# Optimization experiments

Hardware: AMD Instinct MI355X
Metric: run time of the kernel (lower is better)

## Reference

```python
import jax, jax.numpy as jnp
import numpy as np

# irreps layout: in/out = 32x0e + 8x1o  (dim 32 + 24 = 56), sh = 1x0e + 1x1o (dim 4)
NS, NV = 32, 8
N_NODES, N_EDGES, N_EDGE_FEAT, HIDDEN = 10000, 100000, 64, 64
W_NUMEL = NS*NS + NS*NV + NV*NV + NV*NS  # 1600
EPS = 1e-5
# path normalization (e3nn-style 'component'/'element'):
# fan_in into 0e output = 32 (0x0 path) + 8 (1x1 path) = 40; same for 1o output.
INV40 = 1.0 / np.sqrt(40.0)            # paths with trivial/identity CG net factor
INV120 = 1.0 / np.sqrt(120.0)          # paths with w3j = delta/sqrt(3) extra factor


def setup_inputs() -> dict:
    key = jax.random.key(0)
    ks = jax.random.split(key, 12)
    node_attr = jax.random.normal(ks[0], (N_NODES, 56), dtype=jnp.float32)
    edge_attr = jax.random.normal(ks[1], (N_EDGES, N_EDGE_FEAT), dtype=jnp.float32)
    edge_sh = jax.random.normal(ks[2], (N_EDGES, 4), dtype=jnp.float32)
    edge_index = jax.random.randint(ks[3], (2, N_EDGES), 0, N_NODES, dtype=jnp.int64)
    s1 = 1.0 / np.sqrt(N_EDGE_FEAT)
    s2 = 1.0 / np.sqrt(HIDDEN)
    fc1_w = jax.random.normal(ks[4], (N_EDGE_FEAT, HIDDEN), dtype=jnp.float32) * s1
    fc1_b = jnp.zeros((HIDDEN,), dtype=jnp.float32)
    fc2_w = jax.random.normal(ks[5], (HIDDEN, W_NUMEL), dtype=jnp.float32) * s2
    fc2_b = jnp.zeros((W_NUMEL,), dtype=jnp.float32)
    bn_gamma0 = jnp.ones((NS,), dtype=jnp.float32)
    bn_beta0 = jnp.zeros((NS,), dtype=jnp.float32)
    bn_gamma1 = jnp.ones((NV,), dtype=jnp.float32)
    return dict(node_attr=node_attr, edge_attr=edge_attr, edge_sh=edge_sh,
                edge_index=edge_index, fc1_w=fc1_w, fc1_b=fc1_b,
                fc2_w=fc2_w, fc2_b=fc2_b, bn_gamma0=bn_gamma0,
                bn_beta0=bn_beta0, bn_gamma1=bn_gamma1)


def _forward(node_attr, edge_attr, edge_sh, fc1_w, fc1_b, fc2_w, fc2_b,
             bn_gamma0, bn_beta0, bn_gamma1, edge_index):
    E = edge_attr.shape[0]
    N = node_attr.shape[0]
    edge_src, edge_dst = edge_index[0], edge_index[1]

    # edge MLP -> per-edge tensor-product weights [E, 1600]
    h = jax.nn.relu(edge_attr @ fc1_w + fc1_b)
    w = h @ fc2_w + fc2_b
    o1 = NS * NS            # 0e x 0e -> 0e
    o2 = o1 + NS * NV       # 0e x 1o -> 1o
    o3 = o2 + NV * NV       # 1o x 0e -> 1o
    w00 = w[:, :o1].reshape(E, NS, NS)
    w01 = w[:, o1:o2].reshape(E, NS, NV)
    w10 = w[:, o2:o3].reshape(E, NV, NV)
    w11 = w[:, o3:].reshape(E, NV, NS)

    # gather node features at destination, split into scalar / vector irreps
    x = node_attr[edge_dst]                  # [E, 56]
    x0 = x[:, :NS]                           # [E, 32] scalars
    x1 = x[:, NS:].reshape(E, NV, 3)         # [E, 8, 3] l=1 vectors
    s0 = edge_sh[:, 0]                       # [E]
    s1 = edge_sh[:, 1:4]                     # [E, 3]

    # Clebsch-Gordan paths (w3j(1,1,0)=w3j(1,0,1)=w3j(0,1,1)=delta/sqrt(3))
    out0 = jnp.einsum('eu,euw->ew', x0 * s0[:, None], w00) * INV40 \
         + jnp.einsum('eui,ei,euw->ew', x1, s1, w11) * INV120
    out1 = jnp.einsum('eu,ei,euw->ewi', x0, s1, w01) * INV40 \
         + jnp.einsum('eui,euw->ewi', x1 * s0[:, None, None], w10) * INV40
    tp_out = jnp.concatenate([out0, out1.reshape(E, NV * 3)], axis=-1)  # [E, 56]

    # scatter-mean over edge_src
    sums = jax.ops.segment_sum(tp_out, edge_src, num_segments=N)
    cnt = jax.ops.segment_sum(jnp.ones((E,), tp_out.dtype), edge_src, num_segments=N)
    out = sums / jnp.maximum(cnt, 1.0)[:, None]

    # residual (in_dim == out_dim, pad is a no-op)
    out = out + node_attr

    # e3nn-style BatchNorm (training statistics, reduce='mean')
    sc = out[:, :NS]
    vec = out[:, NS:].reshape(N, NV, 3)
    m = sc.mean(axis=0)
    sc_c = sc - m
    var = (sc_c ** 2).mean(axis=0)
    sc_n = sc_c * jax.lax.rsqrt(var + EPS) * bn_gamma0 + bn_beta0
    vnorm = (vec ** 2).mean(axis=-1).mean(axis=0)          # [NV]
    vec_n = vec * (jax.lax.rsqrt(vnorm + EPS) * bn_gamma1)[None, :, None]
    return jnp.concatenate([sc_n, vec_n.reshape(N, NV * 3)], axis=-1)


def reference(node_attr, edge_attr, edge_sh, edge_index, fc1_w, fc1_b,
              fc2_w, fc2_b, bn_gamma0, bn_beta0, bn_gamma1):
    return _forward(node_attr, edge_attr, edge_sh, fc1_w, fc1_b, fc2_w,
                    fc2_b, bn_gamma0, bn_beta0, bn_gamma1, edge_index)
```

## Files before the change

### kernel.cpp

```cpp
#include <hip/hip_runtime.h>

typedef __attribute__((ext_vector_type(4)))  float f32x4;
typedef __attribute__((ext_vector_type(16))) float f32x16;
typedef __attribute__((ext_vector_type(8)))  short bf16x8;
typedef __attribute__((ext_vector_type(4)))  short short4v;

#define NEDGE 100000
#define NNODE 10000
#define INV40f 0.15811388300841897f
#define INV120f 0.09128709291752769f

__device__ inline short f2bf(float f) {
    unsigned u = __builtin_bit_cast(unsigned, f);
    u = (u + 0x7fffu + ((u >> 16) & 1u)) >> 16;
    return (short)u;
}

__device__ __forceinline__ float bperm(int byteIdx, float v) {
    return __builtin_bit_cast(float,
        __builtin_amdgcn_ds_bpermute(byteIdx, __builtin_bit_cast(int, v)));
}

__device__ __forceinline__ void stage16(const void* gsrc, void* ldst) {
    __builtin_amdgcn_global_load_lds(
        (const __attribute__((address_space(1))) unsigned*)gsrc,
        (__attribute__((address_space(3))) unsigned*)(unsigned long long)(uintptr_t)ldst,
        16, 0, 0);
}

#define MFMA32(A,B,C) __builtin_amdgcn_mfma_f32_32x32x16_bf16((A),(B),(C),0,0,0)

__global__ __launch_bounds__(256) void prep(const float* __restrict__ fc1_w,
                                            const float* __restrict__ fc2_w,
                                            short* __restrict__ fc1_wt,
                                            short* __restrict__ fc2_wt,
                                            float* __restrict__ stats,
                                            int* __restrict__ hist) {
    const int b = blockIdx.x, t = threadIdx.x;
    if (b < 25) {
        __shared__ short tile[64 * 66];
        const int c0 = b * 64;
        #pragma unroll
        for (int rep = 0; rep < 16; rep++) {
            const int idx = rep * 256 + t;
            const int k = idx >> 6, c = idx & 63;
            tile[k * 66 + c] = f2bf(fc2_w[(size_t)k * 1600 + c0 + c]);
        }
        __syncthreads();
        short* outp = fc2_wt + b * 4096;
        #pragma unroll
        for (int rep = 0; rep < 16; rep++) {
            const int og = rep * 256 + t;
            const int g2rel = og >> 11;
            const int t2 = (og >> 8) & 7;
            const int cl = ((og >> 3) & 31) + g2rel * 32;
            const int j = og & 7;
            const int k = (t2 >> 1) * 16 + (t2 & 1) * 8 + j;
            outp[og] = tile[k * 66 + cl];
        }
    } else if (b == 25) {
        #pragma unroll
        for (int rep = 0; rep < 16; rep++) {
            const int i = rep * 256 + t;
            fc1_wt[(i & 63) * 64 + (i >> 6)] = f2bf(fc1_w[i]);
        }
    } else if (b == 26) {
        if (t < 72) stats[t] = 0.0f;
    } else {
        const int i = (b - 27) * 256 + t;
        if (i < NNODE) hist[i] = 0;
    }
}

__global__ __launch_bounds__(256, 2) void edge_fused(
    const float* __restrict__ node_attr,
    const float* __restrict__ edge_attr,
    const float* __restrict__ edge_sh,
    const int*   __restrict__ edge_index,
    const float* __restrict__ fc1_b,
    const float* __restrict__ fc2_b,
    const short* __restrict__ fc1_wt,
    const short* __restrict__ fc2_wt,
    float* __restrict__ tp_out,
    int*   __restrict__ hist)
{
    __shared__ __align__(16) char lds[41216];
    char* cbA = lds;
    char* cbB = lds + 16384;
    float* bias_s = (float*)(lds + 34816);

    const int tid  = threadIdx.x;
    const int wid  = tid >> 6;
    const int wtid = tid & 63;
    const int l31  = wtid & 31;
    const int half = wtid >> 5;
    const int e0   = blockIdx.x * 128 + wid * 32;
    const bool active = (e0 < NEDGE);

    char*  h_s = cbB + wid * 4096;
    float* shb = (float*)(lds + 32768 + wid * 512);
    const int swzl = (l31 & 7) << 4;

#define STAGE1(CH, BUF, J) do { \
        const int _o = (wid * 4 + (J)) * 1024 + wtid * 16; \
        stage16((const char*)fc2_wt + (CH) * 16384 + _o, (BUF) + (wid * 4 + (J)) * 1024); \
    } while (0)
#define STAGE_FULL(CH, BUF) do { STAGE1(CH,BUF,0); STAGE1(CH,BUF,1); STAGE1(CH,BUF,2); STAGE1(CH,BUF,3); } while (0)

    STAGE_FULL(0, cbA);

    *(f32x4*)(bias_s + tid * 4) = *(const f32x4*)(fc2_b + tid * 4);
    if (tid < 144)
        *(f32x4*)(bias_s + (tid + 256) * 4) = *(const f32x4*)(fc2_b + (tid + 256) * 4);

    int dst_r = 0;
    if (active && wtid < 32) {
        dst_r = edge_index[NEDGE + e0 + wtid];
        atomicAdd(&hist[edge_index[e0 + wtid]], 1);
        *(f32x4*)(shb + wtid * 4) = *(const f32x4*)(edge_sh + (size_t)(e0 + wtid) * 4);
    }

    bf16x8 hb[4];
    f32x4 shv = {0.f, 0.f, 0.f, 0.f};
    float cb1r[16], c10r[12], c11r[4];
    int vs[2];
    vs[0] = l31 * 4;
    vs[1] = (32 + l31) * 4;

    if (active) {
        const int dstm = __shfl(dst_r, l31, 64);
        const float* nap = node_attr + (size_t)dstm * 56;
        shv = *(const f32x4*)(shb + l31 * 4);

        const f32x4 t0 = *(const f32x4*)(nap + half * 16);
        const f32x4 t1 = *(const f32x4*)(nap + half * 16 + 4);
        const f32x4 t2 = *(const f32x4*)(nap + half * 16 + 8);
        const f32x4 t3 = *(const f32x4*)(nap + half * 16 + 12);
        #pragma unroll
        for (int j = 0; j < 4; j++) {
            cb1r[j]      = INV40f * t0[j];
            cb1r[4 + j]  = INV40f * t1[j];
            cb1r[8 + j]  = INV40f * t2[j];
            cb1r[12 + j] = INV40f * t3[j];
        }
        const f32x4 y0 = *(const f32x4*)(nap + 32 + half * 12);
        const f32x4 y1 = *(const f32x4*)(nap + 32 + half * 12 + 4);
        const f32x4 y2 = *(const f32x4*)(nap + 32 + half * 12 + 8);
        float xx[12];
        #pragma unroll
        for (int j = 0; j < 4; j++) { xx[j] = y0[j]; xx[4 + j] = y1[j]; xx[8 + j] = y2[j]; }
        const float i40s0 = INV40f * shv[0];
        #pragma unroll
        for (int k = 0; k < 12; k++) c10r[k] = i40s0 * xx[k];
        #pragma unroll
        for (int e = 0; e < 4; e++)
            c11r[e] = INV120f * (xx[e*3]*shv[1] + xx[e*3+1]*shv[2] + xx[e*3+2]*shv[3]);

        const float* pe = edge_attr + (size_t)(e0 + l31) * 64 + half * 8;
        bf16x8 eb[4];
        #pragma unroll
        for (int s = 0; s < 4; s++) {
            const f32x4 a = *(const f32x4*)(pe + s * 16);
            const f32x4 b = *(const f32x4*)(pe + s * 16 + 4);
            #pragma unroll
            for (int i = 0; i < 4; i++) { eb[s][i] = f2bf(a[i]); eb[s][4 + i] = f2bf(b[i]); }
        }
        #pragma unroll
        for (int g = 0; g < 2; g++) {
            f32x16 c;
            #pragma unroll
            for (int q = 0; q < 4; q++) {
                const f32x4 bq = *(const f32x4*)(fc1_b + g*32 + q*8 + half*4);
                c[q*4+0] = bq[0]; c[q*4+1] = bq[1]; c[q*4+2] = bq[2]; c[q*4+3] = bq[3];
            }
            #pragma unroll
            for (int s = 0; s < 4; s++) {
                const bf16x8 af = *(const bf16x8*)(fc1_wt + (g*32 + l31)*64 + s*16 + half*8);
                c = MFMA32(af, eb[s], c);
            }
            #pragma unroll
            for (int q = 0; q < 4; q++) {
                short4v p;
                #pragma unroll
                for (int j = 0; j < 4; j++) p[j] = f2bf(fmaxf(c[q*4+j], 0.0f));
                *(short4v*)(h_s + (l31*128 + ((g*64 + q*16 + half*8) ^ swzl))) = p;
            }
        }
        #pragma unroll
        for (int s = 0; s < 4; s++)
            hb[s] = *(const bf16x8*)(h_s + (l31*128 + ((s*32 + half*16) ^ swzl)));
    }

    float acc0[16] = {};
    float ab1[4] = {0,0,0,0};
    float b2[12] = {};

    auto mload = [&](const char* cb, int go, int G) -> f32x16 {
        f32x16 c;
        #pragma unroll
        for (int q = 0; q < 4; q++) {
            const f32x4 bq = *(const f32x4*)(bias_s + G*32 + q*8 + half*4);
            c[q*4+0] = bq[0]; c[q*4+1] = bq[1]; c[q*4+2] = bq[2]; c[q*4+3] = bq[3];
        }
        #pragma unroll
        for (int s = 0; s < 4; s++) {
            const bf16x8 a = *(const bf16x8*)(cb + go*4096 + (s*2 + half)*512 + l31*16);
            c = MFMA32(a, hb[s], c);
        }
        return c;
    };

    auto cons_w00 = [&](const char* cb, int ch) {
        #pragma unroll
        for (int go = 0; go < 4; go++) {
            const int G = ch * 4 + go;
            const f32x16 c = mload(cb, go, G);
            const float cv = shv[0] * bperm(vs[G >> 4], cb1r[G & 15]);
            #pragma unroll
            for (int r = 0; r < 16; r++) acc0[r] += cv * c[r];
        }
    };
    auto cons_w01 = [&](const char* cb, int Gl0) {
        #pragma unroll
        for (int go = 0; go < 4; go++) {
            const int Gl = Gl0 + go;
            const f32x16 c = mload(cb, go, 32 + Gl);
            #pragma unroll
            for (int q = 0; q < 4; q++) {
                const int u = Gl * 4 + q;
                const float cvq = bperm(vs[u >> 4], cb1r[u & 15]);
                #pragma unroll
                for (int j = 0; j < 4; j++) ab1[j] += cvq * c[q*4+j];
            }
        }
    };
    auto cons_w10 = [&](const char* cb) {
        #pragma unroll
        for (int go = 0; go < 2; go++) {
            const f32x16 c = mload(cb, go, 40 + go);
            #pragma unroll
            for (int q = 0; q < 4; q++) {
                const int u = go * 4 + q;
                #pragma unroll
                for (int i = 0; i < 3; i++) {
                    const float cv = bperm(vs[u >> 2], c10r[(u & 3) * 3 + i]);
                    #pragma unroll
                    for (int j = 0; j < 4; j++) b2[j*3+i] += cv * c[q*4+j];
                }
            }
        }
    };
    auto cons_w11_2 = [&](const char* cb, int goBase, int Gl0) {
        #pragma unroll
        for (int go = 0; go < 2; go++) {
            const int Gl = Gl0 + go;
            const f32x16 c = mload(cb, goBase + go, 42 + Gl);
            const float cv = bperm(vs[Gl >> 2], c11r[Gl & 3]);
            #pragma unroll
            for (int r = 0; r < 16; r++) acc0[r] += cv * c[r];
        }
    };
    auto cons_w11_4 = [&](const char* cb, int Gl0) {
        #pragma unroll
        for (int go = 0; go < 4; go++) {
            const int Gl = Gl0 + go;
            const f32x16 c = mload(cb, go, 42 + Gl);
            const float cv = bperm(vs[Gl >> 2], c11r[Gl & 3]);
            #pragma unroll
            for (int r = 0; r < 16; r++) acc0[r] += cv * c[r];
        }
    };

    __syncthreads();
    STAGE_FULL(1,  cbB); if (active) cons_w00(cbA, 0); __syncthreads();
    STAGE_FULL(2,  cbA); if (active) cons_w00(cbB, 1); __syncthreads();
    STAGE_FULL(3,  cbB); if (active) cons_w00(cbA, 2); __syncthreads();
    STAGE_FULL(4,  cbA); if (active) cons_w00(cbB, 3); __syncthreads();
    STAGE_FULL(5,  cbB); if (active) cons_w00(cbA, 4); __syncthreads();
    STAGE_FULL(6,  cbA); if (active) cons_w00(cbB, 5); __syncthreads();
    STAGE_FULL(7,  cbB); if (active) cons_w00(cbA, 6); __syncthreads();
    STAGE_FULL(8,  cbA); if (active) cons_w00(cbB, 7); __syncthreads();
    STAGE_FULL(9,  cbB); if (active) cons_w01(cbA, 0); __syncthreads();
    STAGE_FULL(10, cbA); if (active) cons_w01(cbB, 4); __syncthreads();
    STAGE_FULL(11, cbB); if (active) { cons_w10(cbA); cons_w11_2(cbA, 2, 0); } __syncthreads();
    STAGE_FULL(12, cbA); if (active) cons_w11_4(cbB, 2); __syncthreads();
                         if (active) cons_w11_2(cbA, 0, 6);

    if (!active) return;

    float* orow = tp_out + (size_t)(e0 + l31) * 56;
    #pragma unroll
    for (int q = 0; q < 4; q++)
        *(f32x4*)(orow + q*8 + half*4) = f32x4{acc0[q*4], acc0[q*4+1], acc0[q*4+2], acc0[q*4+3]};
    float ov[12];
    #pragma unroll
    for (int j = 0; j < 4; j++) {
        ov[j*3 + 0] = shv[1] * ab1[j] + b2[j*3 + 0];
        ov[j*3 + 1] = shv[2] * ab1[j] + b2[j*3 + 1];
        ov[j*3 + 2] = shv[3] * ab1[j] + b2[j*3 + 2];
    }
    float* p1 = orow + 32 + half * 12;
    *(f32x4*)(p1)     = f32x4{ov[0], ov[1], ov[2],  ov[3]};
    *(f32x4*)(p1 + 4) = f32x4{ov[4], ov[5], ov[6],  ov[7]};
    *(f32x4*)(p1 + 8) = f32x4{ov[8], ov[9], ov[10], ov[11]};
#undef STAGE1
#undef STAGE_FULL
}

__global__ __launch_bounds__(1024) void scan_hist(const int* __restrict__ hist,
                                                  int* __restrict__ offsets,
                                                  int* __restrict__ cursor) {
    __shared__ int part[1024];
    const int t = threadIdx.x;
    const int n0 = t * 10;
    int lh[10];
    int s = 0;
    if (n0 < NNODE) {
        #pragma unroll
        for (int j = 0; j < 10; j++) { lh[j] = hist[n0 + j]; s += lh[j]; }
    }
    part[t] = s;
    __syncthreads();
    for (int d = 1; d < 1024; d <<= 1) {
        const int v = (t >= d) ? part[t - d] : 0;
        __syncthreads();
        part[t] += v;
        __syncthreads();
    }
    if (n0 < NNODE) {
        int run = part[t] - s;
        #pragma unroll
        for (int j = 0; j < 10; j++) {
            offsets[n0 + j] = run; cursor[n0 + j] = run; run += lh[j];
        }
    }
    if (t == 0) offsets[NNODE] = NEDGE;
}

__global__ __launch_bounds__(256) void fill_perm(const int* __restrict__ edge_index,
                                                 int* __restrict__ cursor,
                                                 int* __restrict__ perm) {
    const int e = blockIdx.x * 256 + threadIdx.x;
    if (e < NEDGE) {
        const int s = edge_index[e];
        const int p = atomicAdd(&cursor[s], 1);
        perm[p] = e;
    }
}

__global__ __launch_bounds__(256) void node_agg(
    const float* __restrict__ tp_out, const int* __restrict__ offsets,
    const int* __restrict__ perm,
    const float* __restrict__ node_attr, float* __restrict__ out,
    float* __restrict__ stats)
{
    __shared__ float part[72];
    const int tid = threadIdx.x;
    if (tid < 72) part[tid] = 0.0f;
    __syncthreads();
    const int n = blockIdx.x * 16 + (tid >> 4);
    const int q = tid & 15;
    if (n < NNODE && q < 14) {
        const int st = offsets[n], en = offsets[n + 1];
        f32x4 acc = {0.f, 0.f, 0.f, 0.f};
        for (int r = st; r < en; r++)
            acc += *(const f32x4*)(tp_out + (size_t)perm[r] * 56 + q * 4);
        const float inv = 1.0f / fmaxf((float)(en - st), 1.0f);
        const int c0 = q * 4;
        const f32x4 res = *(const f32x4*)(node_attr + (size_t)n * 56 + c0);
        f32x4 val;
        #pragma unroll
        for (int j = 0; j < 4; j++) {
            val[j] = acc[j] * inv + res[j];
            const int c = c0 + j;
            if (c < 32) {
                atomicAdd(&part[c], val[j]);
                atomicAdd(&part[32 + c], val[j] * val[j]);
            } else {
                atomicAdd(&part[64 + (c - 32) / 3], val[j] * val[j]);
            }
        }
        *(f32x4*)(out + (size_t)n * 56 + c0) = val;
    }
    __syncthreads();
    if (tid < 72) unsafeAtomicAdd(&stats[tid], part[tid]);
}

__global__ __launch_bounds__(256) void node_norm(
    float* __restrict__ out, const float* __restrict__ stats,
    const float* __restrict__ g0, const float* __restrict__ b0,
    const float* __restrict__ g1)
{
    const int id = blockIdx.x * 256 + threadIdx.x;
    if (id >= NNODE * 56) return;
    const int c = id % 56;
    float val = out[id];
    if (c < 32) {
        const float m   = stats[c]      * (1.0f / NNODE);
        const float ex2 = stats[32 + c] * (1.0f / NNODE);
        const float var = ex2 - m * m;
        val = (val - m) * rsqrtf(var + 1e-5f) * g0[c] + b0[c];
    } else {
        const int v = (c - 32) / 3;
        const float vn = stats[64 + v] * (1.0f / (3.0f * NNODE));
        val = val * rsqrtf(vn + 1e-5f) * g1[v];
    }
    out[id] = val;
}

extern "C" void kernel_launch(void* const* d_in, const int* in_sizes, int n_in,
                              void* d_out, int out_size, void* d_ws, size_t ws_size,
                              hipStream_t stream) {
    const float* node_attr = (const float*)d_in[0];
    const float* edge_attr = (const float*)d_in[1];
    const float* edge_sh   = (const float*)d_in[2];
    const int*   edge_index= (const int*)  d_in[3];
    const float* fc1_w     = (const float*)d_in[4];
    const float* fc1_b     = (const float*)d_in[5];
    const float* fc2_w     = (const float*)d_in[6];
    const float* fc2_b     = (const float*)d_in[7];
    const float* g0        = (const float*)d_in[8];
    const float* b0        = (const float*)d_in[9];
    const float* g1        = (const float*)d_in[10];
    float* out = (float*)d_out;

    char* ws = (char*)d_ws;
    float* stats   = (float*)(ws + 0);
    int*   hist    = (int*)  (ws + 288);
    int*   offsets = (int*)  (ws + 40288);
    int*   cursor  = (int*)  (ws + 80320);
    int*   perm    = (int*)  (ws + 120320);
    short* fc1_wt  = (short*)(ws + 520320);
    short* fc2_wt  = (short*)(ws + 528512);
    float* tp_out  = (float*)(ws + 733312);

    prep<<<67, 256, 0, stream>>>(fc1_w, fc2_w, fc1_wt, fc2_wt, stats, hist);
    edge_fused<<<782, 256, 0, stream>>>(node_attr, edge_attr, edge_sh, edge_index,
                                        fc1_b, fc2_b, fc1_wt, fc2_wt, tp_out, hist);
    scan_hist<<<1, 1024, 0, stream>>>(hist, offsets, cursor);
    fill_perm<<<391, 256, 0, stream>>>(edge_index, cursor, perm);
    node_agg<<<625, 256, 0, stream>>>(tp_out, offsets, perm, node_attr, out, stats);
    node_norm<<<2188, 256, 0, stream>>>(out, stats, g0, b0, g1);
}
```

Baseline: 101.0 us.

## Load fc2 weights directly from global into registers instead of LDS double-buffering

Removes the block-wide global-to-LDS staging of fc2 weight chunks and its per-chunk __syncthreads, and instead has each wave load its MFMA A-operand fragments straight from global/L2 into registers, with a two-deep software prefetch across a single unrolled 50-group loop. LDS use shrinks and the minimum-occupancy hint on launch bounds is dropped. This aims to cut barrier stalls and LDS traffic. The cost is that every wave now reads the same weights from cache separately, and register pressure rises with the prefetch buffers.

```diff
diff --git a/kernel.cpp b/kernel.cpp
--- a/kernel.cpp
+++ b/kernel.cpp
@@ -19,13 +19,6 @@
 __device__ __forceinline__ float bperm(int byteIdx, float v) {
     return __builtin_bit_cast(float,
         __builtin_amdgcn_ds_bpermute(byteIdx, __builtin_bit_cast(int, v)));
-}
-
-__device__ __forceinline__ void stage16(const void* gsrc, void* ldst) {
-    __builtin_amdgcn_global_load_lds(
-        (const __attribute__((address_space(1))) unsigned*)gsrc,
-        (__attribute__((address_space(3))) unsigned*)(unsigned long long)(uintptr_t)ldst,
-        16, 0, 0);
 }
 
 #define MFMA32(A,B,C) __builtin_amdgcn_mfma_f32_32x32x16_bf16((A),(B),(C),0,0,0)
@@ -72,7 +65,7 @@
     }
 }
 
-__global__ __launch_bounds__(256, 2) void edge_fused(
+__global__ __launch_bounds__(256) void edge_fused(
     const float* __restrict__ node_attr,
     const float* __restrict__ edge_attr,
     const float* __restrict__ edge_sh,
@@ -84,10 +77,8 @@
     float* __restrict__ tp_out,
     int*   __restrict__ hist)
 {
-    __shared__ __align__(16) char lds[41216];
-    char* cbA = lds;
-    char* cbB = lds + 16384;
-    float* bias_s = (float*)(lds + 34816);
+    __shared__ __align__(16) char lds[24832];
+    float* bias_s = (float*)(lds + 18432);
 
     const int tid  = threadIdx.x;
     const int wid  = tid >> 6;
@@ -97,17 +88,9 @@
     const int e0   = blockIdx.x * 128 + wid * 32;
     const bool active = (e0 < NEDGE);
 
-    char*  h_s = cbB + wid * 4096;
-    float* shb = (float*)(lds + 32768 + wid * 512);
+    char*  h_s = lds + wid * 4096;
+    float* shb = (float*)(lds + 16384 + wid * 512);
     const int swzl = (l31 & 7) << 4;
-
-#define STAGE1(CH, BUF, J) do { \
-        const int _o = (wid * 4 + (J)) * 1024 + wtid * 16; \
-        stage16((const char*)fc2_wt + (CH) * 16384 + _o, (BUF) + (wid * 4 + (J)) * 1024); \
-    } while (0)
-#define STAGE_FULL(CH, BUF) do { STAGE1(CH,BUF,0); STAGE1(CH,BUF,1); STAGE1(CH,BUF,2); STAGE1(CH,BUF,3); } while (0)
-
-    STAGE_FULL(0, cbA);
 
     *(f32x4*)(bias_s + tid * 4) = *(const f32x4*)(fc2_b + tid * 4);
     if (tid < 144)
@@ -191,40 +174,47 @@
             hb[s] = *(const bf16x8*)(h_s + (l31*128 + ((s*32 + half*16) ^ swzl)));
     }
 
+    __syncthreads();
+
+    if (!active) return;
+
     float acc0[16] = {};
     float ab1[4] = {0,0,0,0};
     float b2[12] = {};
 
-    auto mload = [&](const char* cb, int go, int G) -> f32x16 {
+    const char* wb = (const char*)fc2_wt + half * 512 + l31 * 16;
+    bf16x8 pb[2][4];
+    #pragma unroll
+    for (int s = 0; s < 4; s++) pb[0][s] = *(const bf16x8*)(wb + 0*4096 + s*1024);
+    #pragma unroll
+    for (int s = 0; s < 4; s++) pb[1][s] = *(const bf16x8*)(wb + 1*4096 + s*1024);
+
+    #pragma unroll
+    for (int G = 0; G < 50; ++G) {
+        const int p = G & 1;
+        const bf16x8 w0 = pb[p][0], w1 = pb[p][1], w2 = pb[p][2], w3 = pb[p][3];
+        if (G + 2 < 50) {
+            #pragma unroll
+            for (int s = 0; s < 4; s++)
+                pb[p][s] = *(const bf16x8*)(wb + (G + 2)*4096 + s*1024);
+        }
         f32x16 c;
         #pragma unroll
         for (int q = 0; q < 4; q++) {
             const f32x4 bq = *(const f32x4*)(bias_s + G*32 + q*8 + half*4);
             c[q*4+0] = bq[0]; c[q*4+1] = bq[1]; c[q*4+2] = bq[2]; c[q*4+3] = bq[3];
         }
-        #pragma unroll
-        for (int s = 0; s < 4; s++) {
-            const bf16x8 a = *(const bf16x8*)(cb + go*4096 + (s*2 + half)*512 + l31*16);
-            c = MFMA32(a, hb[s], c);
-        }
-        return c;
-    };
-
-    auto cons_w00 = [&](const char* cb, int ch) {
-        #pragma unroll
-        for (int go = 0; go < 4; go++) {
-            const int G = ch * 4 + go;
-            const f32x16 c = mload(cb, go, G);
+        c = MFMA32(w0, hb[0], c);
+        c = MFMA32(w1, hb[1], c);
+        c = MFMA32(w2, hb[2], c);
+        c = MFMA32(w3, hb[3], c);
+
+        if (G < 32) {
             const float cv = shv[0] * bperm(vs[G >> 4], cb1r[G & 15]);
             #pragma unroll
             for (int r = 0; r < 16; r++) acc0[r] += cv * c[r];
-        }
-    };
-    auto cons_w01 = [&](const char* cb, int Gl0) {
-        #pragma unroll
-        for (int go = 0; go < 4; go++) {
-            const int Gl = Gl0 + go;
-            const f32x16 c = mload(cb, go, 32 + Gl);
+        } else if (G < 40) {
+            const int Gl = G - 32;
             #pragma unroll
             for (int q = 0; q < 4; q++) {
                 const int u = Gl * 4 + q;
@@ -232,12 +222,8 @@
                 #pragma unroll
                 for (int j = 0; j < 4; j++) ab1[j] += cvq * c[q*4+j];
             }
-        }
-    };
-    auto cons_w10 = [&](const char* cb) {
-        #pragma unroll
-        for (int go = 0; go < 2; go++) {
-            const f32x16 c = mload(cb, go, 40 + go);
+        } else if (G < 42) {
+            const int go = G - 40;
             #pragma unroll
             for (int q = 0; q < 4; q++) {
                 const int u = go * 4 + q;
@@ -248,45 +234,13 @@
                     for (int j = 0; j < 4; j++) b2[j*3+i] += cv * c[q*4+j];
                 }
             }
-        }
-    };
-    auto cons_w11_2 = [&](const char* cb, int goBase, int Gl0) {
-        #pragma unroll
-        for (int go = 0; go < 2; go++) {
-            const int Gl = Gl0 + go;
-            const f32x16 c = mload(cb, goBase + go, 42 + Gl);
+        } else {
+            const int Gl = G - 42;
             const float cv = bperm(vs[Gl >> 2], c11r[Gl & 3]);
             #pragma unroll
             for (int r = 0; r < 16; r++) acc0[r] += cv * c[r];
         }
-    };
-    auto cons_w11_4 = [&](const char* cb, int Gl0) {
-        #pragma unroll
-        for (int go = 0; go < 4; go++) {
-            const int Gl = Gl0 + go;
-            const f32x16 c = mload(cb, go, 42 + Gl);
-            const float cv = bperm(vs[Gl >> 2], c11r[Gl & 3]);
-            #pragma unroll
-            for (int r = 0; r < 16; r++) acc0[r] += cv * c[r];
-        }
-    };
-
-    __syncthreads();
-    STAGE_FULL(1,  cbB); if (active) cons_w00(cbA, 0); __syncthreads();
-    STAGE_FULL(2,  cbA); if (active) cons_w00(cbB, 1); __syncthreads();
-    STAGE_FULL(3,  cbB); if (active) cons_w00(cbA, 2); __syncthreads();
-    STAGE_FULL(4,  cbA); if (active) cons_w00(cbB, 3); __syncthreads();
-    STAGE_FULL(5,  cbB); if (active) cons_w00(cbA, 4); __syncthreads();
-    STAGE_FULL(6,  cbA); if (active) cons_w00(cbB, 5); __syncthreads();
-    STAGE_FULL(7,  cbB); if (active) cons_w00(cbA, 6); __syncthreads();
-    STAGE_FULL(8,  cbA); if (active) cons_w00(cbB, 7); __syncthreads();
-    STAGE_FULL(9,  cbB); if (active) cons_w01(cbA, 0); __syncthreads();
-    STAGE_FULL(10, cbA); if (active) cons_w01(cbB, 4); __syncthreads();
-    STAGE_FULL(11, cbB); if (active) { cons_w10(cbA); cons_w11_2(cbA, 2, 0); } __syncthreads();
-    STAGE_FULL(12, cbA); if (active) cons_w11_4(cbB, 2); __syncthreads();
-                         if (active) cons_w11_2(cbA, 0, 6);
-
-    if (!active) return;
+    }
 
     float* orow = tp_out + (size_t)(e0 + l31) * 56;
     #pragma unroll
@@ -303,8 +257,6 @@
     *(f32x4*)(p1)     = f32x4{ov[0], ov[1], ov[2],  ov[3]};
     *(f32x4*)(p1 + 4) = f32x4{ov[4], ov[5], ov[6],  ov[7]};
     *(f32x4*)(p1 + 8) = f32x4{ov[8], ov[9], ov[10], ov[11]};
-#undef STAGE1
-#undef STAGE_FULL
 }
 
 __global__ __launch_bounds__(1024) void scan_hist(const int* __restrict__ hist,
```

Result: slower. 118.1 us (+16.9%).
